# Kernel optimization log

Hardware: AMD Instinct MI355X
Metric: run time of the kernel (lower is better)

## Reference

```python
import jax, jax.numpy as jnp
import numpy as np

N_NODES = 50000
N_EDGES = 800000
DIM = 512
N_CLASSES = 1000


def _xavier(key, shape):
    fan_in, fan_out = shape[0], shape[1]
    lim = float(np.sqrt(6.0 / (fan_in + fan_out)))
    return jax.random.uniform(key, shape, jnp.float32, -lim, lim)


def setup_inputs() -> dict:
    key = jax.random.key(0)
    ks = jax.random.split(key, 12)
    nodes = jax.random.normal(ks[0], (N_NODES, DIM), jnp.float32)
    edges = jax.random.randint(ks[1], (2, N_EDGES), 0, N_NODES, jnp.int64)
    labelmatrix = jax.random.normal(ks[2], (N_CLASSES, 128), jnp.float32)
    return {
        "nodes": nodes,
        "edges": edges,
        "labelmatrix": labelmatrix,
        "W1": _xavier(ks[3], (DIM, 256)), "b1": jnp.zeros((256,), jnp.float32),
        "W2": _xavier(ks[4], (256, 192)), "b2": jnp.zeros((192,), jnp.float32),
        "W3": _xavier(ks[5], (192, 128)), "b3": jnp.zeros((128,), jnp.float32),
        "fc1_w": _xavier(ks[6], (128, 128)), "fc1_b": jnp.zeros((128,), jnp.float32),
        "fc2_w": _xavier(ks[7], (128, 128)), "fc2_b": jnp.zeros((128,), jnp.float32),
    }


def _gcn_conv(x, W, b, src, dst, n):
    # PyG GCNConv: add self-loops, symmetric normalization, then aggregate.
    xw = x @ W                                        # [N, out]
    ones = jnp.ones(src.shape[0], x.dtype)
    deg = jax.ops.segment_sum(ones, dst, num_segments=n) + 1.0  # +1 self-loop
    dinv = jax.lax.rsqrt(deg)                         # deg^{-1/2}
    coef = dinv[src] * dinv[dst]                      # [E]
    agg = jax.ops.segment_sum(xw[src] * coef[:, None], dst, num_segments=n)
    agg = agg + xw * (dinv * dinv)[:, None]           # self-loop contribution
    return agg + b


def reference(nodes, edges, labelmatrix, W1, b1, W2, b2, W3, b3,
              fc1_w, fc1_b, fc2_w, fc2_b):
    src, dst = edges[0], edges[1]
    n = nodes.shape[0]
    # _GraphConv: three stacked GCNConv layers, no inter-layer activation
    x = _gcn_conv(nodes, W1, b1, src, dst, n)
    x = _gcn_conv(x, W2, b2, src, dst, n)
    x = _gcn_conv(x, W3, b3, src, dst, n)             # [N, 128]
    # _GraphLinear (eval mode: dropout is identity)
    h = jax.nn.relu(x @ fc1_w + fc1_b)
    h = h @ fc2_w + fc2_b                             # [N, 128]
    preds = h @ labelmatrix.T                         # dot-product similarity [N, C]
    return preds
```

## Files before the change

kernel.cpp:

```cpp
#include <hip/hip_runtime.h>

typedef unsigned short u16;
typedef __bf16 bf16x8 __attribute__((ext_vector_type(8)));
typedef float f32x4 __attribute__((ext_vector_type(4)));

__device__ __forceinline__ u16 f2bf(float f) {
    unsigned int u = __float_as_uint(f);
    unsigned int r = (u + 0x7FFFu + ((u >> 16) & 1u)) >> 16;
    return (u16)r;
}
__device__ __forceinline__ float bf_lo(unsigned int u) { return __uint_as_float(u << 16); }
__device__ __forceinline__ float bf_hi(unsigned int u) { return __uint_as_float(u & 0xFFFF0000u); }

#define GLOAD_LDS(gp, lp) \
    __builtin_amdgcn_global_load_lds( \
        (const __attribute__((address_space(1))) unsigned int*)(gp), \
        (__attribute__((address_space(3))) unsigned int*)(lp), 16, 0, 0)


__global__ void hist_k(const int* __restrict__ dst, int* __restrict__ deg, int nE) {
    int e = blockIdx.x * 256 + threadIdx.x;
    if (e < nE) atomicAdd(&deg[dst[e]], 1);
}

__global__ void scan_block_k(const int* __restrict__ deg, int* __restrict__ scanned,
                             int* __restrict__ bsums, int n) {
    __shared__ int s[1024];
    int i = blockIdx.x * 1024 + threadIdx.x;
    int v = (i < n) ? deg[i] : 0;
    s[threadIdx.x] = v;
    __syncthreads();
    for (int off = 1; off < 1024; off <<= 1) {
        int t = (threadIdx.x >= off) ? s[threadIdx.x - off] : 0;
        __syncthreads();
        s[threadIdx.x] += t;
        __syncthreads();
    }
    if (i < n) scanned[i] = s[threadIdx.x];
    if (threadIdx.x == 1023) bsums[blockIdx.x] = s[1023];
}

__global__ void scan_sums_k(int* __restrict__ bsums, int nb) {
    int l = threadIdx.x & 63;
    int v = (l < nb) ? bsums[l] : 0;
    int orig = v;
    for (int off = 1; off < 64; off <<= 1) {
        int t = __shfl_up(v, off);
        if (l >= off) v += t;
    }
    if (l < nb) bsums[l] = v - orig;
}

__global__ void scan_final_dinv_k(const int* __restrict__ scanned, const int* __restrict__ deg,
                                  const int* __restrict__ bsums, int* __restrict__ rowptr,
                                  int* __restrict__ wptr, float* __restrict__ dinv,
                                  float* __restrict__ u1, int n, int nE) {
    int i = blockIdx.x * 256 + threadIdx.x;
    if (i < n) {
        int rp = scanned[i] - deg[i] + bsums[i >> 10];
        rowptr[i] = rp;
        wptr[i] = rp;
        float di = rsqrtf((float)deg[i] + 1.0f);
        dinv[i] = di;
        u1[i] = di * di;
    }
    if (i == 0) rowptr[n] = nE;
}

__global__ void csr_fill_k(const int* __restrict__ src, const int* __restrict__ dst,
                           int* __restrict__ wptr, const float* __restrict__ dinv,
                           int* __restrict__ eidx, float* __restrict__ ecoef,
                           float* __restrict__ u1, int nE) {
    int e = blockIdx.x * 256 + threadIdx.x;
    if (e >= nE) return;
    int d = dst[e], s = src[e];
    int p = atomicAdd(&wptr[d], 1);
    float c = dinv[s] * dinv[d];
    eidx[p] = s;
    ecoef[p] = c;
    atomicAdd(&u1[d], c);
}

__global__ void uv2_k(const int* __restrict__ rowptr, const int* __restrict__ eidx,
                      const float* __restrict__ ecoef, const float* __restrict__ dinv,
                      const float* __restrict__ u1, float* __restrict__ u2, int n) {
    int i = blockIdx.x * 256 + threadIdx.x;
    if (i >= n) return;
    float s = dinv[i] * dinv[i] * u1[i];
    int b = rowptr[i], e = rowptr[i + 1];
    for (int k = b; k < e; ++k) s += ecoef[k] * u1[eidx[k]];
    u2[i] = s;
}


__global__ __launch_bounds__(192) void ck1_k(const float* __restrict__ W1,
                                             const float* __restrict__ W2,
                                             float* __restrict__ T1) {
    __shared__ float row[256];
    int i = blockIdx.x;
    for (int t = threadIdx.x; t < 256; t += 192) row[t] = W1[i * 256 + t];
    __syncthreads();
    int j = threadIdx.x;
    float s = 0.f;
    for (int k = 0; k < 256; ++k) s = fmaf(row[k], W2[k * 192 + j], s);
    T1[i * 192 + j] = s;
}

__global__ __launch_bounds__(256) void prep2_k(
    const float* __restrict__ T1, const float* __restrict__ W3, u16* __restrict__ Wp,
    const float* __restrict__ b1, const float* __restrict__ W2, const float* __restrict__ b2,
    float* __restrict__ c1, float* __restrict__ c2,
    const float* __restrict__ fc1_w, u16* __restrict__ Bfc1) {
    __shared__ float sbuf[192];
    const int b = blockIdx.x, tid = threadIdx.x;
    if (b < 512) {
        if (tid < 192) sbuf[tid] = T1[b * 192 + tid];
        __syncthreads();
        if (tid < 128) {
            float s = 0.f;
            for (int m = 0; m < 192; ++m) s = fmaf(sbuf[m], W3[m * 128 + tid], s);
            Wp[(size_t)tid * 512 + b] = f2bf(s);
        }
    } else if (b == 512) {
        if (tid < 192) {
            float s = 0.f;
            for (int k = 0; k < 256; ++k) s = fmaf(b1[k], W2[k * 192 + tid], s);
            sbuf[tid] = s;
        }
        __syncthreads();
        if (tid < 128) {
            float a = 0.f, bb = 0.f;
            for (int m = 0; m < 192; ++m) {
                a  = fmaf(sbuf[m], W3[m * 128 + tid], a);
                bb = fmaf(b2[m],   W3[m * 128 + tid], bb);
            }
            c1[tid] = a; c2[tid] = bb;
        }
    } else {
        int idx = (b - 513) * 256 + tid;
        if (idx < 128 * 128) {
            int nn = idx >> 7, k = idx & 127;
            Bfc1[idx] = f2bf(fc1_w[k * 128 + nn]);
        }
    }
}

__global__ __launch_bounds__(128) void fuse_fc2_k(
    const float* __restrict__ fc2_w, const float* __restrict__ fc2_b,
    const float* __restrict__ labelm, u16* __restrict__ Wc, float* __restrict__ bc) {
    __shared__ float w[128 * 129];
    __shared__ float lm[128];
    __shared__ float red[2];
    const int tid = threadIdx.x;
    for (int t = tid; t < 128 * 128; t += 128)
        w[(t >> 7) * 129 + (t & 127)] = fc2_w[t];
    __syncthreads();
    for (int cc = 0; cc < 8; ++cc) {
        int c = blockIdx.x * 8 + cc;
        lm[tid] = (c < 1000) ? labelm[(size_t)c * 128 + tid] : 0.f;
        __syncthreads();
        float sum = 0.f;
        const float* wr = &w[tid * 129];
        for (int j = 0; j < 128; ++j) sum = fmaf(wr[j], lm[j], sum);
        Wc[(size_t)c * 128 + tid] = f2bf(sum);
        float p = fc2_b[tid] * lm[tid];
        for (int off = 32; off > 0; off >>= 1) p += __shfl_down(p, off);
        if ((tid & 63) == 0) red[tid >> 6] = p;
        __syncthreads();
        if (tid == 0) bc[c] = red[0] + red[1];
        __syncthreads();
    }
}


template <bool CASTA, bool OUTF32, bool BIAS, bool RELU>
__global__ __launch_bounds__(256) void gemm_mfma(
    const void* __restrict__ Ap, const u16* __restrict__ Bt,
    const float* __restrict__ bias, void* __restrict__ Cout,
    int K, int Nout, int ldc, int Mout, int lgny, int Arows) {
    __shared__ __align__(16) u16 As[128 * 64];
    __shared__ __align__(16) u16 Bs[128 * 64];
    const int tid  = threadIdx.x;
    const int lane = tid & 63;
    const int w    = tid >> 6;
    const int wm   = w >> 1, wn = w & 1;

    const int nwg = gridDim.x, orig = blockIdx.x;
    const int q = nwg >> 3, r = nwg & 7;
    const int xcd = orig & 7, off = orig >> 3;
    const int tile = (xcd < r ? xcd * (q + 1) : r * (q + 1) + (xcd - r) * q) + off;
    const int ny = 1 << lgny;
    const int tx = tile >> lgny, ty = tile & (ny - 1);
    const size_t bm = (size_t)tx * 128;
    const size_t bn = (size_t)ty * 128;

    const int l7 = lane & 7;
    const int l3 = lane >> 3;
    const int kcs = l7 ^ l3;

    f32x4 acc[4][4] = {};

    for (int k0 = 0; k0 < K; k0 += 64) {
        if constexpr (CASTA) {
            const float* Af = (const float*)Ap;
            const int row = tid >> 1;
            const int half = tid & 1;
            const size_t grow = bm + row;
            const bool valid = grow < (size_t)Arows;
            const float4* g4 = (const float4*)(Af + grow * K + k0 + half * 32);
            float4 f[8];
#pragma unroll
            for (int j = 0; j < 8; ++j)
                f[j] = valid ? g4[j] : make_float4(0.f, 0.f, 0.f, 0.f);
#pragma unroll
            for (int j = 0; j < 4; ++j) {
                int kc = (half * 4 + j) ^ (row & 7);
                uint4 o;
                o.x = (unsigned)f2bf(f[2 * j].x)     | ((unsigned)f2bf(f[2 * j].y) << 16);
                o.y = (unsigned)f2bf(f[2 * j].z)     | ((unsigned)f2bf(f[2 * j].w) << 16);
                o.z = (unsigned)f2bf(f[2 * j + 1].x) | ((unsigned)f2bf(f[2 * j + 1].y) << 16);
                o.w = (unsigned)f2bf(f[2 * j + 1].z) | ((unsigned)f2bf(f[2 * j + 1].w) << 16);
                *(uint4*)((char*)As + row * 128 + kc * 16) = o;
            }
#pragma unroll
            for (int it = 0; it < 4; ++it) {
                const int r0 = w * 32 + it * 8;
                const u16* gB = Bt + ((size_t)(bn + r0 + l3) * K + k0) + kcs * 8;
                GLOAD_LDS(gB, Bs + r0 * 64);
            }
        } else {
            const u16* A = (const u16*)Ap;
#pragma unroll
            for (int it = 0; it < 4; ++it) {
                const int r0 = w * 32 + it * 8;
                const u16* gA = A + ((size_t)(bm + r0 + l3) * K + k0) + kcs * 8;
                GLOAD_LDS(gA, As + r0 * 64);
                const u16* gB = Bt + ((size_t)(bn + r0 + l3) * K + k0) + kcs * 8;
                GLOAD_LDS(gB, Bs + r0 * 64);
            }
        }
        __syncthreads();

#pragma unroll
        for (int ks = 0; ks < 2; ++ks) {
            bf16x8 av[4], bv[4];
#pragma unroll
            for (int i = 0; i < 4; ++i) {
                int row = wm * 64 + i * 16 + (lane & 15);
                int kc = (ks * 4 + (lane >> 4)) ^ (lane & 7);
                av[i] = *(const bf16x8*)((const char*)As + row * 128 + kc * 16);
            }
#pragma unroll
            for (int j = 0; j < 4; ++j) {
                int nn = wn * 64 + j * 16 + (lane & 15);
                int kc = (ks * 4 + (lane >> 4)) ^ (lane & 7);
                bv[j] = *(const bf16x8*)((const char*)Bs + nn * 128 + kc * 16);
            }
#pragma unroll
            for (int i = 0; i < 4; ++i)
#pragma unroll
                for (int j = 0; j < 4; ++j)
                    acc[i][j] = __builtin_amdgcn_mfma_f32_16x16x32_bf16(av[i], bv[j], acc[i][j], 0, 0, 0);
        }
        __syncthreads();
    }

    const int ccol  = lane & 15;
    const int crow4 = (lane >> 4) * 4;
#pragma unroll
    for (int i = 0; i < 4; ++i) {
#pragma unroll
        for (int j = 0; j < 4; ++j) {
#pragma unroll
            for (int r2 = 0; r2 < 4; ++r2) {
                size_t gr = bm + wm * 64 + i * 16 + crow4 + r2;
                size_t gc = bn + wn * 64 + j * 16 + ccol;
                if (gr < (size_t)Mout && gc < (size_t)Nout) {
                    float v = acc[i][j][r2];
                    if constexpr (BIAS) v += bias[gc];
                    if constexpr (RELU) v = fmaxf(v, 0.f);
                    if constexpr (OUTF32) ((float*)Cout)[gr * ldc + gc] = v;
                    else                  ((u16*)Cout)[gr * ldc + gc] = f2bf(v);
                }
            }
        }
    }
}


template <bool FINAL>
__global__ __launch_bounds__(256) void aggw_k(
    const u16* __restrict__ xw, const int* __restrict__ rowptr,
    const int* __restrict__ eidx, const float* __restrict__ ecoef,
    const float* __restrict__ dinv, u16* __restrict__ out,
    const float* __restrict__ u1v, const float* __restrict__ u2v,
    const float* __restrict__ c1, const float* __restrict__ c2,
    const float* __restrict__ b3, int n) {
    const int lane = threadIdx.x & 63;
    const int wave = threadIdx.x >> 6;
    const int g = lane >> 4, fl = lane & 15;
    const int node = blockIdx.x * 4 + wave;
    if (node >= n) return;
    const uint4* xv = (const uint4*)xw;

    float acc[8] = {};
    const int beg = rowptr[node], end = rowptr[node + 1];
    for (int e0 = beg; e0 < end; e0 += 16) {
#pragma unroll
        for (int qq = 0; qq < 4; ++qq) {
            int ee = e0 + qq * 4 + g;
            int sn = node; float c = 0.f;
            if (ee < end) { sn = eidx[ee]; c = ecoef[ee]; }
            uint4 v = xv[(size_t)sn * 16 + fl];
            acc[0] = fmaf(c, bf_lo(v.x), acc[0]); acc[1] = fmaf(c, bf_hi(v.x), acc[1]);
            acc[2] = fmaf(c, bf_lo(v.y), acc[2]); acc[3] = fmaf(c, bf_hi(v.y), acc[3]);
            acc[4] = fmaf(c, bf_lo(v.z), acc[4]); acc[5] = fmaf(c, bf_hi(v.z), acc[5]);
            acc[6] = fmaf(c, bf_lo(v.w), acc[6]); acc[7] = fmaf(c, bf_hi(v.w), acc[7]);
        }
    }
#pragma unroll
    for (int k = 0; k < 8; ++k) {
        acc[k] += __shfl_xor(acc[k], 16);
        acc[k] += __shfl_xor(acc[k], 32);
    }
    if (g == 0) {
        float di = dinv[node];
        float s = di * di;
        uint4 a = xv[(size_t)node * 16 + fl];
        acc[0] = fmaf(s, bf_lo(a.x), acc[0]); acc[1] = fmaf(s, bf_hi(a.x), acc[1]);
        acc[2] = fmaf(s, bf_lo(a.y), acc[2]); acc[3] = fmaf(s, bf_hi(a.y), acc[3]);
        acc[4] = fmaf(s, bf_lo(a.z), acc[4]); acc[5] = fmaf(s, bf_hi(a.z), acc[5]);
        acc[6] = fmaf(s, bf_lo(a.w), acc[6]); acc[7] = fmaf(s, bf_hi(a.w), acc[7]);
        if constexpr (FINAL) {
            float uu1 = u1v[node], uu2 = u2v[node];
            float4 c1a = ((const float4*)c1)[fl * 2], c1b = ((const float4*)c1)[fl * 2 + 1];
            float4 c2a = ((const float4*)c2)[fl * 2], c2b = ((const float4*)c2)[fl * 2 + 1];
            float4 b3a = ((const float4*)b3)[fl * 2], b3b = ((const float4*)b3)[fl * 2 + 1];
            acc[0] += uu2 * c1a.x + uu1 * c2a.x + b3a.x;
            acc[1] += uu2 * c1a.y + uu1 * c2a.y + b3a.y;
            acc[2] += uu2 * c1a.z + uu1 * c2a.z + b3a.z;
            acc[3] += uu2 * c1a.w + uu1 * c2a.w + b3a.w;
            acc[4] += uu2 * c1b.x + uu1 * c2b.x + b3b.x;
            acc[5] += uu2 * c1b.y + uu1 * c2b.y + b3b.y;
            acc[6] += uu2 * c1b.z + uu1 * c2b.z + b3b.z;
            acc[7] += uu2 * c1b.w + uu1 * c2b.w + b3b.w;
        }
        uint4 o;
        o.x = (unsigned)f2bf(acc[0]) | ((unsigned)f2bf(acc[1]) << 16);
        o.y = (unsigned)f2bf(acc[2]) | ((unsigned)f2bf(acc[3]) << 16);
        o.z = (unsigned)f2bf(acc[4]) | ((unsigned)f2bf(acc[5]) << 16);
        o.w = (unsigned)f2bf(acc[6]) | ((unsigned)f2bf(acc[7]) << 16);
        ((uint4*)out)[(size_t)node * 16 + fl] = o;
    }
}


extern "C" void kernel_launch(void* const* d_in, const int* in_sizes, int n_in,
                              void* d_out, int out_size, void* d_ws, size_t ws_size,
                              hipStream_t stream) {
    const float* nodes  = (const float*)d_in[0];
    const int*   edges  = (const int*)d_in[1];
    const float* labelm = (const float*)d_in[2];
    const float* W1 = (const float*)d_in[3];
    const float* b1 = (const float*)d_in[4];
    const float* W2 = (const float*)d_in[5];
    const float* b2 = (const float*)d_in[6];
    const float* W3 = (const float*)d_in[7];
    const float* b3 = (const float*)d_in[8];
    const float* fc1_w = (const float*)d_in[9];
    const float* fc1_b = (const float*)d_in[10];
    const float* fc2_w = (const float*)d_in[11];
    const float* fc2_b = (const float*)d_in[12];
    float* out = (float*)d_out;

    const int DIM = 512, N3 = 128, NC = 1000;
    const int n  = in_sizes[0] / DIM;
    const int nE = in_sizes[1] / 2;
    const int Mpad = 50048;
    const int* src = edges;
    const int* dst = edges + nE;

    u16* Y = (u16*)((char*)d_out + 67108864);
    u16* Z = (u16*)((char*)d_out + 100663296);

    char* ws = (char*)d_ws;
    u16*   Q      = (u16*)(ws);
    u16*   Rb     = (u16*)(ws + 12812288);
    float* T1     = (float*)(ws + 25624576);
    u16*   Wp     = (u16*)(ws + 26017792);
    u16*   Bfc1   = (u16*)(ws + 26148864);
    u16*   Wc     = (u16*)(ws + 26181632);
    float* bc     = (float*)(ws + 26443776);
    float* c1     = (float*)(ws + 26447872);
    float* c2     = (float*)(ws + 26448384);
    float* u1     = (float*)(ws + 26448896);
    float* u2     = (float*)(ws + 26648896);
    int*   deg_i  = (int*)(ws + 26848896);
    float* dinv   = (float*)(ws + 27048896);
    int*   rowptr = (int*)(ws + 27248896);
    int*   wptr   = (int*)(ws + 27448960);
    int*   scanned= (int*)(ws + 27648960);
    int*   bsums  = (int*)(ws + 27848960);
    int*   eidx   = (int*)(ws + 27849216);
    float* ecoef  = (float*)(ws + 31049216);

    hipMemsetAsync(deg_i, 0, (size_t)n * 4, stream);
    hist_k<<<(nE + 255) / 256, 256, 0, stream>>>(dst, deg_i, nE);
    int nb = (n + 1023) / 1024;
    scan_block_k<<<nb, 1024, 0, stream>>>(deg_i, scanned, bsums, n);
    scan_sums_k<<<1, 64, 0, stream>>>(bsums, nb);
    scan_final_dinv_k<<<(n + 255) / 256, 256, 0, stream>>>(scanned, deg_i, bsums, rowptr, wptr, dinv, u1, n, nE);
    csr_fill_k<<<(nE + 255) / 256, 256, 0, stream>>>(src, dst, wptr, dinv, eidx, ecoef, u1, nE);
    uv2_k<<<(n + 255) / 256, 256, 0, stream>>>(rowptr, eidx, ecoef, dinv, u1, u2, n);

    ck1_k<<<512, 192, 0, stream>>>(W1, W2, T1);
    prep2_k<<<577, 256, 0, stream>>>(T1, W3, Wp, b1, W2, b2, c1, c2, fc1_w, Bfc1);
    fuse_fc2_k<<<128, 128, 0, stream>>>(fc2_w, fc2_b, labelm, Wc, bc);

    const int gx = Mpad / 128;
    dim3 blk(256);
    const int gagg = (n + 3) / 4;

    gemm_mfma<true, false, false, false><<<gx, blk, 0, stream>>>(nodes, Wp, nullptr, Y, 512, N3, N3, Mpad, 0, n);
    aggw_k<false><<<gagg, blk, 0, stream>>>(Y, rowptr, eidx, ecoef, dinv, Z, nullptr, nullptr, nullptr, nullptr, nullptr, n);
    aggw_k<false><<<gagg, blk, 0, stream>>>(Z, rowptr, eidx, ecoef, dinv, Y, nullptr, nullptr, nullptr, nullptr, nullptr, n);
    aggw_k<true ><<<gagg, blk, 0, stream>>>(Y, rowptr, eidx, ecoef, dinv, Rb, u1, u2, c1, c2, b3, n);
    gemm_mfma<false, false, true, true><<<gx, blk, 0, stream>>>(Rb, Bfc1, fc1_b, Q, 128, N3, N3, Mpad, 0, Mpad);
    gemm_mfma<false, true, true, false><<<gx * 8, blk, 0, stream>>>(Q, Wc, bc, out, 128, NC, NC, n, 3, Mpad);
}
```

Before: 427.9 us.

## Map one 16-lane group per node in aggregation with 8-way unrolled gathers

The aggregation kernel now assigns 16 threads per node (16 nodes per block) instead of one 64-lane wave per node split into four edge groups. This removes the cross-group shuffle reduction and the idle lanes in the epilogue. The edge loop is unrolled by 8 with index and coefficient loads batched before the row gathers, which raises memory-level parallelism per thread. The cost is divergence inside a wave, since four nodes with different degrees share one wave.

```diff
diff --git a/kernel.cpp b/kernel.cpp
--- a/kernel.cpp
+++ b/kernel.cpp
@@ -289,69 +289,76 @@
 
 
 template <bool FINAL>
-__global__ __launch_bounds__(256) void aggw_k(
+__global__ __launch_bounds__(256) void agg128_k(
     const u16* __restrict__ xw, const int* __restrict__ rowptr,
     const int* __restrict__ eidx, const float* __restrict__ ecoef,
     const float* __restrict__ dinv, u16* __restrict__ out,
     const float* __restrict__ u1v, const float* __restrict__ u2v,
     const float* __restrict__ c1, const float* __restrict__ c2,
     const float* __restrict__ b3, int n) {
-    const int lane = threadIdx.x & 63;
-    const int wave = threadIdx.x >> 6;
-    const int g = lane >> 4, fl = lane & 15;
-    const int node = blockIdx.x * 4 + wave;
+    const int tid = threadIdx.x;
+    const int sub = tid >> 4;
+    const int fl  = tid & 15;
+    int node = blockIdx.x * 16 + sub;
     if (node >= n) return;
+
     const uint4* xv = (const uint4*)xw;
-
-    float acc[8] = {};
+    float di = dinv[node];
+    float s = di * di;
+    uint4 a = xv[(size_t)node * 16 + fl];
+    float acc[8];
+    acc[0] = s * bf_lo(a.x); acc[1] = s * bf_hi(a.x);
+    acc[2] = s * bf_lo(a.y); acc[3] = s * bf_hi(a.y);
+    acc[4] = s * bf_lo(a.z); acc[5] = s * bf_hi(a.z);
+    acc[6] = s * bf_lo(a.w); acc[7] = s * bf_hi(a.w);
+
     const int beg = rowptr[node], end = rowptr[node + 1];
-    for (int e0 = beg; e0 < end; e0 += 16) {
-#pragma unroll
-        for (int qq = 0; qq < 4; ++qq) {
-            int ee = e0 + qq * 4 + g;
-            int sn = node; float c = 0.f;
-            if (ee < end) { sn = eidx[ee]; c = ecoef[ee]; }
-            uint4 v = xv[(size_t)sn * 16 + fl];
-            acc[0] = fmaf(c, bf_lo(v.x), acc[0]); acc[1] = fmaf(c, bf_hi(v.x), acc[1]);
-            acc[2] = fmaf(c, bf_lo(v.y), acc[2]); acc[3] = fmaf(c, bf_hi(v.y), acc[3]);
-            acc[4] = fmaf(c, bf_lo(v.z), acc[4]); acc[5] = fmaf(c, bf_hi(v.z), acc[5]);
-            acc[6] = fmaf(c, bf_lo(v.w), acc[6]); acc[7] = fmaf(c, bf_hi(v.w), acc[7]);
-        }
-    }
-#pragma unroll
-    for (int k = 0; k < 8; ++k) {
-        acc[k] += __shfl_xor(acc[k], 16);
-        acc[k] += __shfl_xor(acc[k], 32);
-    }
-    if (g == 0) {
-        float di = dinv[node];
-        float s = di * di;
-        uint4 a = xv[(size_t)node * 16 + fl];
-        acc[0] = fmaf(s, bf_lo(a.x), acc[0]); acc[1] = fmaf(s, bf_hi(a.x), acc[1]);
-        acc[2] = fmaf(s, bf_lo(a.y), acc[2]); acc[3] = fmaf(s, bf_hi(a.y), acc[3]);
-        acc[4] = fmaf(s, bf_lo(a.z), acc[4]); acc[5] = fmaf(s, bf_hi(a.z), acc[5]);
-        acc[6] = fmaf(s, bf_lo(a.w), acc[6]); acc[7] = fmaf(s, bf_hi(a.w), acc[7]);
-        if constexpr (FINAL) {
-            float uu1 = u1v[node], uu2 = u2v[node];
-            float4 c1a = ((const float4*)c1)[fl * 2], c1b = ((const float4*)c1)[fl * 2 + 1];
-            float4 c2a = ((const float4*)c2)[fl * 2], c2b = ((const float4*)c2)[fl * 2 + 1];
-            float4 b3a = ((const float4*)b3)[fl * 2], b3b = ((const float4*)b3)[fl * 2 + 1];
-            acc[0] += uu2 * c1a.x + uu1 * c2a.x + b3a.x;
-            acc[1] += uu2 * c1a.y + uu1 * c2a.y + b3a.y;
-            acc[2] += uu2 * c1a.z + uu1 * c2a.z + b3a.z;
-            acc[3] += uu2 * c1a.w + uu1 * c2a.w + b3a.w;
-            acc[4] += uu2 * c1b.x + uu1 * c2b.x + b3b.x;
-            acc[5] += uu2 * c1b.y + uu1 * c2b.y + b3b.y;
-            acc[6] += uu2 * c1b.z + uu1 * c2b.z + b3b.z;
-            acc[7] += uu2 * c1b.w + uu1 * c2b.w + b3b.w;
-        }
-        uint4 o;
-        o.x = (unsigned)f2bf(acc[0]) | ((unsigned)f2bf(acc[1]) << 16);
-        o.y = (unsigned)f2bf(acc[2]) | ((unsigned)f2bf(acc[3]) << 16);
-        o.z = (unsigned)f2bf(acc[4]) | ((unsigned)f2bf(acc[5]) << 16);
-        o.w = (unsigned)f2bf(acc[6]) | ((unsigned)f2bf(acc[7]) << 16);
-        ((uint4*)out)[(size_t)node * 16 + fl] = o;
-    }
+    int e = beg;
+    for (; e + 7 < end; e += 8) {
+        int sn[8]; float cf[8]; uint4 v[8];
+#pragma unroll
+        for (int q = 0; q < 8; ++q) { sn[q] = eidx[e + q]; cf[q] = ecoef[e + q]; }
+#pragma unroll
+        for (int q = 0; q < 8; ++q) v[q] = xv[(size_t)sn[q] * 16 + fl];
+#pragma unroll
+        for (int q = 0; q < 8; ++q) {
+            acc[0] = fmaf(cf[q], bf_lo(v[q].x), acc[0]); acc[1] = fmaf(cf[q], bf_hi(v[q].x), acc[1]);
+            acc[2] = fmaf(cf[q], bf_lo(v[q].y), acc[2]); acc[3] = fmaf(cf[q], bf_hi(v[q].y), acc[3]);
+            acc[4] = fmaf(cf[q], bf_lo(v[q].z), acc[4]); acc[5] = fmaf(cf[q], bf_hi(v[q].z), acc[5]);
+            acc[6] = fmaf(cf[q], bf_lo(v[q].w), acc[6]); acc[7] = fmaf(cf[q], bf_hi(v[q].w), acc[7]);
+        }
+    }
+    for (; e < end; ++e) {
+        int sn = eidx[e];
+        float c = ecoef[e];
+        uint4 v = xv[(size_t)sn * 16 + fl];
+        acc[0] = fmaf(c, bf_lo(v.x), acc[0]); acc[1] = fmaf(c, bf_hi(v.x), acc[1]);
+        acc[2] = fmaf(c, bf_lo(v.y), acc[2]); acc[3] = fmaf(c, bf_hi(v.y), acc[3]);
+        acc[4] = fmaf(c, bf_lo(v.z), acc[4]); acc[5] = fmaf(c, bf_hi(v.z), acc[5]);
+        acc[6] = fmaf(c, bf_lo(v.w), acc[6]); acc[7] = fmaf(c, bf_hi(v.w), acc[7]);
+    }
+
+    if constexpr (FINAL) {
+        float uu1 = u1v[node], uu2 = u2v[node];
+        float4 c1a = ((const float4*)c1)[fl * 2], c1b = ((const float4*)c1)[fl * 2 + 1];
+        float4 c2a = ((const float4*)c2)[fl * 2], c2b = ((const float4*)c2)[fl * 2 + 1];
+        float4 b3a = ((const float4*)b3)[fl * 2], b3b = ((const float4*)b3)[fl * 2 + 1];
+        acc[0] += uu2 * c1a.x + uu1 * c2a.x + b3a.x;
+        acc[1] += uu2 * c1a.y + uu1 * c2a.y + b3a.y;
+        acc[2] += uu2 * c1a.z + uu1 * c2a.z + b3a.z;
+        acc[3] += uu2 * c1a.w + uu1 * c2a.w + b3a.w;
+        acc[4] += uu2 * c1b.x + uu1 * c2b.x + b3b.x;
+        acc[5] += uu2 * c1b.y + uu1 * c2b.y + b3b.y;
+        acc[6] += uu2 * c1b.z + uu1 * c2b.z + b3b.z;
+        acc[7] += uu2 * c1b.w + uu1 * c2b.w + b3b.w;
+    }
+
+    uint4 o;
+    o.x = (unsigned)f2bf(acc[0]) | ((unsigned)f2bf(acc[1]) << 16);
+    o.y = (unsigned)f2bf(acc[2]) | ((unsigned)f2bf(acc[3]) << 16);
+    o.z = (unsigned)f2bf(acc[4]) | ((unsigned)f2bf(acc[5]) << 16);
+    o.w = (unsigned)f2bf(acc[6]) | ((unsigned)f2bf(acc[7]) << 16);
+    ((uint4*)out)[(size_t)node * 16 + fl] = o;
 }
 
 
@@ -419,12 +426,12 @@
 
     const int gx = Mpad / 128;
     dim3 blk(256);
-    const int gagg = (n + 3) / 4;
+    const int gagg = (n + 15) / 16;
 
     gemm_mfma<true, false, false, false><<<gx, blk, 0, stream>>>(nodes, Wp, nullptr, Y, 512, N3, N3, Mpad, 0, n);
-    aggw_k<false><<<gagg, blk, 0, stream>>>(Y, rowptr, eidx, ecoef, dinv, Z, nullptr, nullptr, nullptr, nullptr, nullptr, n);
-    aggw_k<false><<<gagg, blk, 0, stream>>>(Z, rowptr, eidx, ecoef, dinv, Y, nullptr, nullptr, nullptr, nullptr, nullptr, n);
-    aggw_k<true ><<<gagg, blk, 0, stream>>>(Y, rowptr, eidx, ecoef, dinv, Rb, u1, u2, c1, c2, b3, n);
+    agg128_k<false><<<gagg, blk, 0, stream>>>(Y, rowptr, eidx, ecoef, dinv, Z, nullptr, nullptr, nullptr, nullptr, nullptr, n);
+    agg128_k<false><<<gagg, blk, 0, stream>>>(Z, rowptr, eidx, ecoef, dinv, Y, nullptr, nullptr, nullptr, nullptr, nullptr, n);
+    agg128_k<true ><<<gagg, blk, 0, stream>>>(Y, rowptr, eidx, ecoef, dinv, Rb, u1, u2, c1, c2, b3, n);
     gemm_mfma<false, false, true, true><<<gx, blk, 0, stream>>>(Rb, Bfc1, fc1_b, Q, 128, N3, N3, Mpad, 0, Mpad);
     gemm_mfma<false, true, true, false><<<gx * 8, blk, 0, stream>>>(Q, Wc, bc, out, 128, NC, NC, n, 3, Mpad);
 }
```

Result: no change. 428.0 us (+0.0%).
